# Kernel optimization log

Hardware: AMD Instinct MI355X
Metric: run time of the kernel (lower is better)

## Reference

```python
import jax, jax.numpy as jnp
import numpy as np
import math
from jax import lax

NUM_POS = 128        # random_choice in pos_neg_sampling
NUM_TOT = 256        # pos + (128 + negative_padding) always totals 256
POS_W = 10.0         # positive_weight in compute_loss


def _conv(x, w, b, pad):
    y = lax.conv_general_dilated(x, w, (1, 1), pad,
                                 dimension_numbers=('NCHW', 'OIHW', 'NCHW'))
    return y + b[None, :, None, None]


def make_anchor_box(img_h, img_w, gh, gw):
    # torch.range(0, W, W/(gw-1)) == inclusive linspace with gw points
    xs = jnp.linspace(0.0, float(img_w), gw)
    ys = jnp.linspace(0.0, float(img_h), gh)
    gx, gy = jnp.meshgrid(xs, ys, indexing='ij')          # (gw, gh) like torch.meshgrid
    xy = jnp.stack([gx.reshape(-1), gy.reshape(-1)], -1).reshape(gh, gw, 2)
    whs = []
    for area in (128 * 128, 256 * 256, 512 * 512):
        for wr, hr in ((1, 1), (2, 1), (1, 2)):
            u = math.sqrt(area / (wr * hr))
            whs.append((wr * u, hr * u))
    wh = jnp.asarray(whs, jnp.float32)                    # (9, 2)
    xy9 = jnp.broadcast_to(xy[:, :, None, :], (gh, gw, 9, 2))
    wh9 = jnp.broadcast_to(wh[None, None], (gh, gw, 9, 2))
    boxes = jnp.concatenate([xy9, xy9 + wh9], -1)         # x1,y1,x2,y2
    return boxes.reshape(-1, 4)


def pairwise_iou(t, a):
    # t: [T,4], a: [A,4], xyxy -> [T,A]
    lt = jnp.maximum(t[:, None, :2], a[None, :, :2])
    rb = jnp.minimum(t[:, None, 2:], a[None, :, 2:])
    wh = jnp.clip(rb - lt, 0.0)
    inter = wh[..., 0] * wh[..., 1]
    at = (t[:, 2] - t[:, 0]) * (t[:, 3] - t[:, 1])
    aa = (a[:, 2] - a[:, 0]) * (a[:, 3] - a[:, 1])
    return inter / (at[:, None] + aa[None, :] - inter)


def box_encode(anchor, bbox):
    awh = anchor[:, 2:] - anchor[:, :2]
    bwh = bbox[:, 2:] - bbox[:, :2]
    ac = anchor[:, :2] + awh / 2
    bc = bbox[:, :2] + bwh / 2
    dxy = (bc - ac) / awh
    dwh = jnp.log(bwh / awh)
    return jnp.concatenate([dxy, dwh], 1)


def rpn_forward(x, target, conv_w, conv_b, bbox_w, bbox_b, score_w, score_b,
                img_h, img_w):
    gh, gw = x.shape[-2], x.shape[-1]
    h = jax.nn.relu(_conv(x[None], conv_w, conv_b, 'SAME'))
    bbox = jax.nn.relu(_conv(h, bbox_w, bbox_b, 'VALID')).reshape(-1, 4)   # [A,4]
    score = jax.nn.relu(_conv(h, score_w, score_b, 'VALID')).reshape(-1, 2)  # [A,2]
    anchors = make_anchor_box(img_h, img_w, gh, gw)                        # [A,4]

    iou = pairwise_iou(target, anchors)                                    # [T,A]
    max_iou = iou.max(0)
    tgt_idx = jnp.argmax(iou, 0)

    # deterministic replacement for np.random.choice sampling (fixed shapes)
    pos_score = jnp.where(max_iou > 0.7, max_iou, -1.0)
    pos_vals, pos_idx = lax.top_k(pos_score, NUM_POS)
    pos_valid = pos_vals > 0.0
    n_pos = jnp.sum(pos_valid.astype(jnp.int32))

    neg_score = jnp.where(max_iou < 0.3, 1.0 - max_iou, -1.0)
    neg_vals, neg_idx = lax.top_k(neg_score, NUM_TOT)
    neg_valid = (neg_vals > 0.0) & (jnp.arange(NUM_TOT) < (NUM_TOT - n_pos))

    bbox_pred = bbox[pos_idx]                                              # [128,4]
    scores_sel = score[jnp.concatenate([pos_idx, neg_idx])]                # [384,2]
    valid = jnp.concatenate([pos_valid, neg_valid]).astype(jnp.float32)

    tgt_scores = jnp.concatenate([
        jnp.tile(jnp.asarray([[1.0, 0.0]], jnp.float32), (NUM_POS, 1)),
        jnp.tile(jnp.asarray([[0.0, 1.0]], jnp.float32), (NUM_TOT, 1))], 0)

    matched = target[tgt_idx[pos_idx]]
    treg = box_encode(anchors[pos_idx], matched)

    ce = -jnp.sum(tgt_scores * jax.nn.log_softmax(scores_sel, -1), -1)
    score_loss = jnp.sum(ce * valid) / jnp.maximum(jnp.sum(valid), 1.0)

    d = bbox_pred - treg
    sl1 = jnp.where(jnp.abs(d) < 1.0, 0.5 * d * d, jnp.abs(d) - 0.5)
    pm = pos_valid.astype(jnp.float32)[:, None]
    reg_loss = jnp.sum(sl1 * pm) / jnp.maximum(jnp.sum(pm) * 4.0, 1.0)

    return score_loss + POS_W * reg_loss


def setup_inputs():
    key = jax.random.key(0)
    ks = jax.random.split(key, 8)
    cin, gh, gw, nt = 512, 128, 128, 64
    x = jax.random.normal(ks[0], (cin, gh, gw), jnp.float32)
    cxy = jax.random.uniform(ks[1], (nt, 2), minval=300.0, maxval=1748.0)
    wh = jax.random.uniform(ks[2], (nt, 2), minval=64.0, maxval=512.0)
    target = jnp.concatenate([cxy - wh / 2, cxy + wh / 2], -1)
    conv_w = jax.random.normal(ks[3], (cin, cin, 3, 3), jnp.float32) * 0.02
    conv_b = jnp.zeros((cin,), jnp.float32)
    bbox_w = jax.random.normal(ks[4], (36, cin, 1, 1), jnp.float32) * 0.02
    bbox_b = jnp.zeros((36,), jnp.float32)
    score_w = jax.random.normal(ks[5], (18, cin, 1, 1), jnp.float32) * 0.02
    score_b = jnp.zeros((18,), jnp.float32)
    return {'x': x, 'target': target, 'conv_w': conv_w, 'conv_b': conv_b,
            'bbox_w': bbox_w, 'bbox_b': bbox_b, 'score_w': score_w,
            'score_b': score_b, 'img_h': 2048, 'img_w': 2048}


def reference(x, target, conv_w, conv_b, bbox_w, bbox_b, score_w, score_b,
              img_h, img_w):
    return rpn_forward(x, target, conv_w, conv_b, bbox_w, bbox_b,
                       score_w, score_b, img_h, img_w)
```

## Files before the change

kernel.cpp:

```cpp
#include <hip/hip_runtime.h>
#include <cstdint>
#include <cstddef>

typedef unsigned long long ull;
typedef __bf16 bf16x8 __attribute__((ext_vector_type(8)));
typedef float f32x4 __attribute__((ext_vector_type(4)));

#define NA     147456
#define NT     64
#define KDIM   4608
#define NTASK  1280
#define CAND_CAP 4096
#define KSPLIT 8
#define NSTEP  18
#define NIOUB  576
#define NTRB   2048
#define NPREP2 512
#define NZERO  197

#define OFF_WB2   0
#define OFF_XT    4718592
#define OFF_ZERO  22024192
#define OFF_H4    22302720
#define OFF_MIOU  43274240
#define OFF_CAND  43864064
#define OFF_CPB   45043712
#define OFF_CBZ   45046016
#define OFF_NPOS  45048320
#define OFF_TREG  45048336
#define OFF_TASKS 45050384

#define UANC 90.509667991878f
__device__ __constant__ float WKa[9] = {128.0f, 2.0f*UANC, UANC, 256.0f, 4.0f*UANC, 2.0f*UANC, 512.0f, 8.0f*UANC, 4.0f*UANC};
__device__ __constant__ float HKa[9] = {128.0f, UANC, 2.0f*UANC, 256.0f, 2.0f*UANC, 4.0f*UANC, 512.0f, 4.0f*UANC, 8.0f*UANC};

__device__ __forceinline__ float iou_one(float x1, float y1, float x2, float y2, float4 t) {
#pragma clang fp contract(off)
  float ltx = fmaxf(t.x, x1), lty = fmaxf(t.y, y1);
  float rbx = fminf(t.z, x2), rby = fminf(t.w, y2);
  float wx = fmaxf(rbx - ltx, 0.0f);
  float wy = fmaxf(rby - lty, 0.0f);
  float inter = wx * wy;
  float at = (t.z - t.x) * (t.w - t.y);
  float aa = (x2 - x1) * (y2 - y1);
  return inter / ((at + aa) - inter);
}

__device__ __forceinline__ unsigned short f2bf(float f) {
  unsigned int u = __float_as_uint(f);
  unsigned int r = (u + 0x7fffu + ((u >> 16) & 1u)) >> 16;
  return (unsigned short)r;
}

__device__ __forceinline__ int boff(int kcb) {
  int rk = kcb >> 6;
  int dy = (rk * 11) >> 5;
  int dxo = rk - dy * 3;
  return (dy * 130 + dxo) * 512 + (kcb & 63) * 8;
}

__global__ __launch_bounds__(256) void k_pi(const float* __restrict__ cw,
    unsigned short* __restrict__ Wb2, const float* __restrict__ x,
    unsigned short* __restrict__ xtb, unsigned short* __restrict__ zrg,
    const float* __restrict__ tgt, const int* __restrict__ imw,
    const int* __restrict__ imh, float* __restrict__ miou,
    ull* __restrict__ cand, int* __restrict__ cpb, int* __restrict__ cbz,
    float* __restrict__ out0) {
  __shared__ __align__(16) char smem[20480];
  int blk = blockIdx.x;
  int tid = threadIdx.x;
  if (blk >= NIOUB + NTRB + NPREP2) {
    int g = (blk - (NIOUB + NTRB + NPREP2)) * 256 + tid;
    uint4 z = {0u, 0u, 0u, 0u};
    if (g == 0) *out0 = 0.0f;
    if (g < 17408) {
      *(uint4*)(zrg + g * 8) = z;
    } else {
      int h = g - 17408;
      int pixi = h >> 6, j = h & 63;
      int yy, xx;
      if (pixi < 260) { yy = (pixi < 130) ? 0 : 129; xx = (pixi < 130) ? pixi : pixi - 130; }
      else { int p2 = pixi - 260; if (p2 < 128) { yy = 1 + p2; xx = 0; } else { yy = p2 - 127; xx = 129; } }
      *(uint4*)(xtb + (size_t)(yy * 130 + xx) * 512 + j * 8) = z;
    }
    return;
  }
  if (blk >= NIOUB + NTRB) {
    float* row = (float*)smem;
    int m = blk - (NIOUB + NTRB);
    const float* src = cw + (size_t)m * KDIM;
    for (int f = tid; f < KDIM; f += 256) {
      int cin = f / 9;
      row[cin * 10 + (f - cin * 9)] = src[f];
    }
    __syncthreads();
    for (int kc = tid; kc < 576; kc += 256) {
      int r = kc >> 6, c8 = kc & 63;
      int base = c8 * 80 + r;
      unsigned short o[8];
      #pragma unroll
      for (int j = 0; j < 8; ++j) o[j] = f2bf(row[base + j * 10]);
      *(uint4*)(Wb2 + ((size_t)kc * 512 + m) * 8) = *(const uint4*)o;
    }
    return;
  }
  if (blk >= NIOUB) {
    float* tile = (float*)smem;
    int tb = blk - NIOUB;
    int pix0 = (tb & 255) * 64;
    int cin0 = (tb >> 8) * 64;
    int pr = tid & 15, cr = tid >> 4;
    #pragma unroll
    for (int i = 0; i < 4; ++i) {
      int cin = cr + i * 16;
      float4 v = *(const float4*)(x + (size_t)(cin0 + cin) * 16384 + pix0 + pr * 4);
      tile[cin * 65 + pr * 4 + 0] = v.x;
      tile[cin * 65 + pr * 4 + 1] = v.y;
      tile[cin * 65 + pr * 4 + 2] = v.z;
      tile[cin * 65 + pr * 4 + 3] = v.w;
    }
    __syncthreads();
    #pragma unroll
    for (int i = 0; i < 4; ++i) {
      int pix = cr + i * 16;
      int plin = pix0 + pix;
      int py = plin >> 7, px = plin & 127;
      unsigned short o[4] = {f2bf(tile[(pr * 4 + 0) * 65 + pix]),
                             f2bf(tile[(pr * 4 + 1) * 65 + pix]),
                             f2bf(tile[(pr * 4 + 2) * 65 + pix]),
                             f2bf(tile[(pr * 4 + 3) * 65 + pix])};
      *(uint2*)(xtb + (size_t)((py + 1) * 130 + (px + 1)) * 512 + cin0 + pr * 4) = *(const uint2*)o;
    }
    return;
  }
  float4* ts = (float4*)smem;
  int* wz = (int*)(smem + 1024);
  int* wc = wz + 4;
  if (tid < NT) ts[tid] = ((const float4*)tgt)[tid];
  __syncthreads();
  int a = blk * 256 + tid;
  int k = a % 9;
  int pq = a / 9;
  int p = pq >> 7, q = pq & 127;
  float dx = (float)(*imw) / 127.0f;
  float dyl = (float)(*imh) / 127.0f;
  float x1 = (float)p * dx, y1 = (float)q * dyl;
  float x2 = x1 + WKa[k], y2 = y1 + HKa[k];
  float best = -1.0f;
  #pragma unroll 8
  for (int t = 0; t < NT; ++t) best = fmaxf(best, iou_one(x1, y1, x2, y2, ts[t]));
  miou[a] = best;
  int lane = tid & 63, w = tid >> 6;
  ull bz = __ballot(best == 0.0f);
  bool isc = best > 0.7f;
  ull bc = __ballot(isc);
  if (lane == 0) { wz[w] = (int)__popcll(bz); wc[w] = (int)__popcll(bc); }
  __syncthreads();
  if (tid == 0) {
    cbz[blk] = wz[0] + wz[1] + wz[2] + wz[3];
    cpb[blk] = wc[0] + wc[1] + wc[2] + wc[3];
  }
  if (isc) {
    int woff = 0;
    for (int i = 0; i < w; ++i) woff += wc[i];
    int rank = woff + (int)__popcll(bc & ((1ull << lane) - 1ull));
    cand[blk * 256 + rank] = ((ull)__float_as_uint(best) << 32) | (ull)(0xFFFFFFFFu - (unsigned)a);
  }
}

__global__ __launch_bounds__(256) void k_sel(const ull* __restrict__ cand,
    const int* __restrict__ cpb, const float* __restrict__ miou,
    const int* __restrict__ cbz, const float* __restrict__ tgt,
    const int* __restrict__ imw, const int* __restrict__ imh,
    int* __restrict__ nposp, float* __restrict__ treg, int* __restrict__ tasks) {
  __shared__ ull keys[CAND_CAP];
  __shared__ ull bnd[1024];
  __shared__ int hist[1024];
  __shared__ int cpbL[576];
  __shared__ int base576[577];
  __shared__ int wtot[4];
  __shared__ int selCnt, bndCnt, Tbin, mAbove;
  __shared__ int posi[128];
  __shared__ int npS;
  __shared__ int nzbase[145];
  __shared__ float4 ts[NT];
  __shared__ int negA[256];
  __shared__ int wsum[4];
  int tid = threadIdx.x;
  int lane = tid & 63;
  if (tid < NT) ts[tid] = ((const float4*)tgt)[tid];
  for (int i = tid; i < 576; i += 256) cpbL[i] = cpb[i];
  for (int i = tid; i < 1024; i += 256) hist[i] = 0;
  __syncthreads();
  int e0 = 0, e1 = 0, sA = 0, scanA = 0;
  if (tid < 192) {
    e0 = cpbL[3 * tid]; e1 = cpbL[3 * tid + 1]; int e2 = cpbL[3 * tid + 2];
    sA = e0 + e1 + e2;
    scanA = sA;
    for (int off = 1; off < 64; off <<= 1) {
      int v = __shfl_up(scanA, off);
      if (lane >= off) scanA += v;
    }
    if (lane == 63) wtot[tid >> 6] = scanA;
  }
  __syncthreads();
  if (tid < 192) {
    int w = tid >> 6;
    int woff = 0;
    for (int i = 0; i < w; ++i) woff += wtot[i];
    int excl = woff + scanA - sA;
    base576[3 * tid]     = excl;
    base576[3 * tid + 1] = excl + e0;
    base576[3 * tid + 2] = excl + e0 + e1;
    if (tid == 191) base576[576] = excl + sA;
  }
  __syncthreads();
  int cnt = base576[576]; if (cnt > CAND_CAP) cnt = CAND_CAP;
  for (int i = tid; i < CAND_CAP; i += 256) if (i >= cnt) keys[i] = 0ull;
  for (int rk = tid; rk < cnt; rk += 256) {
    int lo = 0, hi = 576;
    while (hi - lo > 1) { int mid = (lo + hi) >> 1; if (base576[mid] <= rk) lo = mid; else hi = mid; }
    keys[rk] = cand[lo * 256 + (rk - base576[lo])];
  }
  __syncthreads();
  if (cnt <= 128) {
    if (tid < cnt) posi[tid] = (int)(0xFFFFFFFFu - (unsigned)(keys[tid] & 0xFFFFFFFFull));
    if (tid == 0) { npS = cnt; *nposp = cnt; }
  } else {
    for (int i = tid; i < cnt; i += 256) {
      unsigned ib = (unsigned)(keys[i] >> 32);
      atomicAdd(&hist[(ib - 0x3F333334u) >> 13], 1);
    }
    __syncthreads();
    if (tid < 64) {
      int s = 0;
      #pragma unroll
      for (int t = 0; t < 16; ++t) s += hist[tid * 16 + t];
      int S = s;
      #pragma unroll
      for (int off = 1; off < 64; off <<= 1) {
        int u = __shfl_down(S, off);
        if (tid + off < 64) S += u;
      }
      ull mask = __ballot(S >= 128);
      int g = 63 - __clzll(mask);
      int aboveS = __shfl(S, (g + 1 < 64) ? g + 1 : 63);
      if (g == 63) aboveS = 0;
      if (tid == 0) {
        int run = aboveS, T = g * 16 + 15;
        for (int b = g * 16 + 15; b >= g * 16; --b) {
          int h = hist[b];
          if (run + h >= 128) { T = b; break; }
          run += h;
        }
        Tbin = T; mAbove = run; selCnt = 0; bndCnt = 0;
      }
    }
    __syncthreads();
    int T = Tbin, m = mAbove;
    for (int i = tid; i < cnt; i += 256) {
      ull kk = keys[i];
      unsigned ib = (unsigned)(kk >> 32);
      int b = (int)((ib - 0x3F333334u) >> 13);
      if (b > T) {
        int r = atomicAdd(&selCnt, 1);
        posi[r] = (int)(0xFFFFFFFFu - (unsigned)(kk & 0xFFFFFFFFull));
      } else if (b == T) {
        int r = atomicAdd(&bndCnt, 1);
        if (r < 1024) bnd[r] = kk;
      }
    }
    __syncthreads();
    int B = bndCnt;
    int need = 128 - m;
    if (B <= 1024) {
      int n2 = 2; while (n2 < B) n2 <<= 1;
      for (int i = tid; i < n2; i += 256) if (i >= B) bnd[i] = 0ull;
      for (int size = 2; size <= n2; size <<= 1)
        for (int stride = size >> 1; stride > 0; stride >>= 1) {
          __syncthreads();
          for (int t = tid; t < n2 / 2; t += 256) {
            int i = 2 * t - (t & (stride - 1));
            int j = i + stride;
            ull a = bnd[i], b2 = bnd[j];
            bool desc = ((i & size) == 0);
            if (desc ? (a < b2) : (a > b2)) { bnd[i] = b2; bnd[j] = a; }
          }
        }
      __syncthreads();
      if (tid < need) posi[m + tid] = (int)(0xFFFFFFFFu - (unsigned)(bnd[tid] & 0xFFFFFFFFull));
    } else {
      for (int size = 2; size <= CAND_CAP; size <<= 1)
        for (int stride = size >> 1; stride > 0; stride >>= 1) {
          __syncthreads();
          for (int t = tid; t < CAND_CAP / 2; t += 256) {
            int i = 2 * t - (t & (stride - 1));
            int j = i + stride;
            ull a = keys[i], b2 = keys[j];
            bool desc = ((i & size) == 0);
            if (desc ? (a < b2) : (a > b2)) { keys[i] = b2; keys[j] = a; }
          }
        }
      __syncthreads();
      if (tid < 128) posi[tid] = (int)(0xFFFFFFFFu - (unsigned)(keys[tid] & 0xFFFFFFFFull));
    }
    if (tid == 0) { npS = 128; *nposp = 128; }
  }
  __syncthreads();
  int np = npS;
  int sB = 0, scanB = 0;
  if (tid < 144) {
    int4 cz4 = *(const int4*)(cbz + 4 * tid);
    sB = cz4.x + cz4.y + cz4.z + cz4.w;
    scanB = sB;
    for (int off = 1; off < 64; off <<= 1) {
      int v = __shfl_up(scanB, off);
      if (lane >= off) scanB += v;
    }
    bool last = (tid < 128) ? (lane == 63) : (tid == 143);
    if (last) wsum[tid >> 6] = scanB;
  }
  __syncthreads();
  if (tid < 144) {
    int w = tid >> 6;
    int woff = 0;
    for (int i = 0; i < w; ++i) woff += wsum[i];
    nzbase[tid] = woff + scanB - sB;
    if (tid == 143) nzbase[144] = woff + scanB;
  }
  __syncthreads();
  int w = tid >> 6;
  for (int j = 0; j < 144; ++j) {
    if (nzbase[j] >= 256) break;
    int a0 = j * 1024 + tid * 4;
    float4 m4 = *(const float4*)(miou + a0);
    int f0 = (m4.x == 0.0f), f1 = (m4.y == 0.0f), f2 = (m4.z == 0.0f), f3 = (m4.w == 0.0f);
    int tsum = f0 + f1 + f2 + f3;
    int scan = tsum;
    for (int off = 1; off < 64; off <<= 1) {
      int v = __shfl_up(scan, off);
      if (lane >= off) scan += v;
    }
    if (lane == 63) wsum[w] = scan;
    __syncthreads();
    int woff = nzbase[j];
    for (int i = 0; i < w; ++i) woff += wsum[i];
    int r = woff + scan - tsum;
    if (f0) { if (r < 256) negA[r] = a0;     r++; }
    if (f1) { if (r < 256) negA[r] = a0 + 1; r++; }
    if (f2) { if (r < 256) negA[r] = a0 + 2; r++; }
    if (f3) { if (r < 256) negA[r] = a0 + 3;      }
    __syncthreads();
  }
  __syncthreads();
  if (tid < np) {
    int a = posi[tid];
    int k = a % 9; int pq = a / 9; int p = pq >> 7, q = pq & 127;
    float dx = (float)(*imw) / 127.0f, dyl = (float)(*imh) / 127.0f;
    float x1 = (float)p * dx, y1 = (float)q * dyl;
    float x2 = x1 + WKa[k], y2 = y1 + HKa[k];
    float best = -1.0f; int bt = 0;
    for (int t = 0; t < NT; ++t) {
      float v = iou_one(x1, y1, x2, y2, ts[t]);
      if (v > best) { best = v; bt = t; }
    }
    float4 m = ts[bt];
    float aw = x2 - x1, ah = y2 - y1;
    float acx = x1 + aw * 0.5f, acy = y1 + ah * 0.5f;
    float bwd = m.z - m.x, bhd = m.w - m.y;
    float bcx = m.x + bwd * 0.5f, bcy = m.y + bhd * 0.5f;
    treg[tid * 4 + 0] = (bcx - acx) / aw;
    treg[tid * 4 + 1] = (bcy - acy) / ah;
    treg[tid * 4 + 2] = logf(bwd / aw);
    treg[tid * 4 + 3] = logf(bhd / ah);
  }
  for (int t = tid; t < NTASK; t += 256) {
    int rec = 0;
    if (t < 768) {
      int s = t / 6, jj = t - s * 6;
      if (s < np) {
        int a = posi[s];
        int f, wr, xx;
        if (jj < 4) { f = 4 * a; wr = f >> 14; xx = (f & 127) + jj; }
        else        { f = 2 * a; wr = 36 + (f >> 14); xx = (f & 127) + (jj - 4); }
        int yy = (f >> 7) & 127;
        rec = (int)(0x80000000u | ((unsigned)wr << 16) | ((unsigned)yy << 8) | (unsigned)xx);
      }
    } else {
      int s = (t - 768) >> 1, jj = (t - 768) & 1;
      if (s < 256 - np) {
        int a = negA[s];
        int f = 2 * a; int wr = 36 + (f >> 14); int yy = (f >> 7) & 127; int xx = (f & 127) + jj;
        rec = (int)(0x80000000u | ((unsigned)wr << 16) | ((unsigned)yy << 8) | (unsigned)xx);
      }
    }
    tasks[t] = rec;
  }
}

__global__ __launch_bounds__(64) void k_mfma(const unsigned short* __restrict__ Wb2,
    const unsigned short* __restrict__ xtb, const unsigned short* __restrict__ zrg,
    const int* __restrict__ tasks, const int* __restrict__ nposp,
    float* __restrict__ H4) {
  int npos = *nposp;
  int tt0 = blockIdx.x * 64;
  int posend = 6 * npos, negend = 768 + 2 * (256 - npos);
  if (!((tt0 < posend) || ((tt0 + 64 > 768) && (tt0 < negend)))) return;
  int m_base = blockIdx.y * 64;
  int ks = blockIdx.z;
  int lane = threadIdx.x;
  int quad = lane >> 4, r = lane & 15;
  int kc0 = ks * 72 + quad;
  const bf16x8* Ab = (const bf16x8*)Wb2 + ((size_t)kc0 * 512 + m_base + r);

  const unsigned short* Bp[4];
  #pragma unroll
  for (int ni = 0; ni < 4; ++ni) {
    int rec = tasks[tt0 + ni * 16 + r];
    int pix = (rec < 0) ? (((rec >> 8) & 127) * 130 + (rec & 127)) : 0;
    const unsigned short* base = (rec < 0) ? xtb : zrg;
    Bp[ni] = base + (size_t)pix * 512 + quad * 8;
  }
  int kcb = ks * 72;

  f32x4 acc[4][4];
  #pragma unroll
  for (int i = 0; i < 4; ++i)
    #pragma unroll
    for (int j = 0; j < 4; ++j) acc[i][j] = (f32x4){0.f, 0.f, 0.f, 0.f};

  bf16x8 a[4], b[4];
  #pragma unroll
  for (int mi = 0; mi < 4; ++mi) a[mi] = Ab[mi * 16];
  int ob0 = boff(kcb);
  #pragma unroll
  for (int ni = 0; ni < 4; ++ni) b[ni] = *(const bf16x8*)(Bp[ni] + ob0);

  for (int s = 0; s < NSTEP; ++s) {
    bf16x8 an[4], bn[4];
    if (s < NSTEP - 1) {
      const bf16x8* An = Ab + (size_t)(s + 1) * 4 * 512;
      int ob = boff(kcb + 4 * (s + 1));
      #pragma unroll
      for (int mi = 0; mi < 4; ++mi) an[mi] = An[mi * 16];
      #pragma unroll
      for (int ni = 0; ni < 4; ++ni) bn[ni] = *(const bf16x8*)(Bp[ni] + ob);
    }
    #pragma unroll
    for (int mi = 0; mi < 4; ++mi)
      #pragma unroll
      for (int ni = 0; ni < 4; ++ni)
        acc[mi][ni] = __builtin_amdgcn_mfma_f32_16x16x32_bf16(a[mi], b[ni], acc[mi][ni], 0, 0, 0);
    if (s < NSTEP - 1) {
      #pragma unroll
      for (int mi = 0; mi < 4; ++mi) a[mi] = an[mi];
      #pragma unroll
      for (int ni = 0; ni < 4; ++ni) b[ni] = bn[ni];
    }
  }
  size_t hb = (size_t)ks * NTASK;
  #pragma unroll
  for (int mi = 0; mi < 4; ++mi) {
    int c = m_base + mi * 16 + quad * 4;
    #pragma unroll
    for (int ni = 0; ni < 4; ++ni) {
      int t = tt0 + ni * 16 + r;
      *(f32x4*)(H4 + (hb + t) * 512 + c) = acc[mi][ni];
    }
  }
}

__global__ __launch_bounds__(256) void k_out(const float* __restrict__ H4,
    const int* __restrict__ tasks,
    const float* __restrict__ cb, const float* __restrict__ bw,
    const float* __restrict__ bb, const float* __restrict__ sw,
    const float* __restrict__ sb, const float* __restrict__ treg,
    const int* __restrict__ nposp, float* __restrict__ out) {
  __shared__ float sOut[4];
  __shared__ float sContrib[4];
  int wave = threadIdx.x >> 6, lane = threadIdx.x & 63;
  int t = blockIdx.x * 4 + wave;
  int rec = tasks[t];
  float outval = 0.0f;
  if (rec < 0) {
    int wr = (rec >> 16) & 63;
    const float* wrow = (wr < 36) ? (bw + wr * 512) : (sw + (wr - 36) * 512);
    float s = 0.0f;
    #pragma unroll
    for (int it = 0; it < 8; ++it) {
      int c = it * 64 + lane;
      size_t o = (size_t)t * 512 + c;
      float hv = cb[c];
      #pragma unroll
      for (int kslice = 0; kslice < KSPLIT; ++kslice)
        hv += H4[o + (size_t)kslice * 1280 * 512];
      s = fmaf(fmaxf(hv, 0.0f), wrow[c], s);
    }
    #pragma unroll
    for (int off = 32; off > 0; off >>= 1) s += __shfl_down(s, off);
    if (lane == 0) {
      float b = (wr < 36) ? bb[wr] : sb[wr - 36];
      outval = fmaxf(s + b, 0.0f);
    }
  }
  if (lane == 0) sOut[wave] = outval;
  __syncthreads();
  if (lane == 0) {
    float contrib = 0.0f;
    if (rec < 0) {
      if (t < 768) {
        int s6 = t / 6, j = t - s6 * 6;
        if (j < 4) {
          int np = *nposp;
          float d = outval - treg[s6 * 4 + j];
          float ad = fabsf(d);
          float sl1 = (ad < 1.0f) ? 0.5f * d * d : ad - 0.5f;
          contrib = 10.0f * sl1 / fmaxf(4.0f * (float)np, 1.0f);
        } else if (j == 4) {
          float s0 = outval, s1 = sOut[wave + 1];
          float mm = fmaxf(s0, s1);
          float lse = mm + logf(expf(s0 - mm) + expf(s1 - mm));
          contrib = (lse - s0) * (1.0f / 256.0f);
        }
      } else if (((t - 768) & 1) == 0) {
        float s0 = outval, s1 = sOut[wave + 1];
        float mm = fmaxf(s0, s1);
        float lse = mm + logf(expf(s0 - mm) + expf(s1 - mm));
        contrib = (lse - s1) * (1.0f / 256.0f);
      }
    }
    sContrib[wave] = contrib;
  }
  __syncthreads();
  if (threadIdx.x == 0) {
    float c = sContrib[0] + sContrib[1] + sContrib[2] + sContrib[3];
    if (c != 0.0f) atomicAdd(out, c);
  }
}

extern "C" void kernel_launch(void* const* d_in, const int* in_sizes, int n_in,
                              void* d_out, int out_size, void* d_ws, size_t ws_size,
                              hipStream_t stream) {
  const float* x   = (const float*)d_in[0];
  const float* tgt = (const float*)d_in[1];
  const float* cw  = (const float*)d_in[2];
  const float* cb  = (const float*)d_in[3];
  const float* bw  = (const float*)d_in[4];
  const float* bb  = (const float*)d_in[5];
  const float* sw  = (const float*)d_in[6];
  const float* sb  = (const float*)d_in[7];
  const int* imh   = (const int*)d_in[8];
  const int* imw   = (const int*)d_in[9];

  char* ws = (char*)d_ws;
  unsigned short* Wb2 = (unsigned short*)(ws + OFF_WB2);
  unsigned short* xtb = (unsigned short*)(ws + OFF_XT);
  unsigned short* zrg = (unsigned short*)(ws + OFF_ZERO);
  float* H4    = (float*)(ws + OFF_H4);
  float* miou  = (float*)(ws + OFF_MIOU);
  ull*   cand  = (ull*)(ws + OFF_CAND);
  int*   cpb   = (int*)(ws + OFF_CPB);
  int*   cbz   = (int*)(ws + OFF_CBZ);
  int*   nposp = (int*)(ws + OFF_NPOS);
  float* treg  = (float*)(ws + OFF_TREG);
  int*   tasks = (int*)(ws + OFF_TASKS);
  float* out   = (float*)d_out;

  k_pi   <<<dim3(NIOUB + NTRB + NPREP2 + NZERO), dim3(256), 0, stream>>>(cw, Wb2, x, xtb, zrg, tgt, imw, imh, miou, cand, cpb, cbz, out);
  k_sel  <<<dim3(1),              dim3(256), 0, stream>>>(cand, cpb, miou, cbz, tgt, imw, imh, nposp, treg, tasks);
  k_mfma <<<dim3(20, 8, KSPLIT),  dim3(64),  0, stream>>>(Wb2, xtb, zrg, tasks, nposp, H4);
  k_out  <<<dim3(320),            dim3(256), 0, stream>>>(H4, tasks, cb, bw, bb, sw, sb, treg, nposp, out);
}
```

Before: 149.8 us.

## Fuse selection kernel into prep kernel via block-0 spin-wait on IoU counter

Removes the single-block k_sel launch and runs its selection logic in block 0 of k_pi. That block spin-waits on a global counter that the IoU blocks increment after a threadfence. Selection can then overlap with the transpose and weight-prep blocks of the same kernel, and one launch gap disappears. In exchange it adds a memset, reads candidate keys from global memory through a binary search on each use instead of caching them in shared memory, and relies on block 0 being co-resident with the IoU blocks to avoid deadlock.

```diff
diff --git a/kernel.cpp b/kernel.cpp
--- a/kernel.cpp
+++ b/kernel.cpp
@@ -29,6 +29,7 @@
 #define OFF_NPOS  45048320
 #define OFF_TREG  45048336
 #define OFF_TASKS 45050384
+#define OFF_CTR   45055504
 
 #define UANC 90.509667991878f
 __device__ __constant__ float WKa[9] = {128.0f, 2.0f*UANC, UANC, 256.0f, 4.0f*UANC, 2.0f*UANC, 512.0f, 8.0f*UANC, 4.0f*UANC};
@@ -59,16 +60,253 @@
   return (dy * 130 + dxo) * 512 + (kcb & 63) * 8;
 }
 
+__device__ __forceinline__ ull fetch_key(const ull* __restrict__ cand,
+                                         const int* base576, int rk) {
+  int lo = 0, hi = 576;
+  while (hi - lo > 1) { int mid = (lo + hi) >> 1; if (base576[mid] <= rk) lo = mid; else hi = mid; }
+  return cand[lo * 256 + (rk - base576[lo])];
+}
+
 __global__ __launch_bounds__(256) void k_pi(const float* __restrict__ cw,
     unsigned short* __restrict__ Wb2, const float* __restrict__ x,
     unsigned short* __restrict__ xtb, unsigned short* __restrict__ zrg,
     const float* __restrict__ tgt, const int* __restrict__ imw,
     const int* __restrict__ imh, float* __restrict__ miou,
     ull* __restrict__ cand, int* __restrict__ cpb, int* __restrict__ cbz,
-    float* __restrict__ out0) {
+    float* __restrict__ out0, int* __restrict__ nposp, float* __restrict__ treg,
+    int* __restrict__ tasks, int* __restrict__ ctr, ull* __restrict__ gscr) {
   __shared__ __align__(16) char smem[20480];
-  int blk = blockIdx.x;
+  int blk0 = blockIdx.x;
   int tid = threadIdx.x;
+
+  if (blk0 == 0) {
+    ull* bnd      = (ull*)smem;
+    int* hist     = (int*)(smem + 8192);
+    int* cpbL     = (int*)(smem + 12288);
+    int* base576  = (int*)(smem + 14592);
+    int* wtot     = (int*)(smem + 16900);
+    int* posi     = (int*)(smem + 16916);
+    int* nzbase   = (int*)(smem + 17428);
+    float4* ts    = (float4*)(smem + 18016);
+    int* negA     = (int*)(smem + 19040);
+    int* wsum     = (int*)(smem + 20064);
+    int* scal     = (int*)(smem + 20080);
+    int &selCnt = scal[0], &bndCnt = scal[1], &Tbin = scal[2], &mAbove = scal[3], &npS = scal[4];
+
+    if (tid == 0) {
+      while (atomicCAS(ctr, NIOUB, NIOUB) != NIOUB) __builtin_amdgcn_s_sleep(32);
+    }
+    __syncthreads();
+    __threadfence();
+
+    int lane = tid & 63;
+    if (tid < NT) ts[tid] = ((const float4*)tgt)[tid];
+    for (int i = tid; i < 576; i += 256) cpbL[i] = cpb[i];
+    for (int i = tid; i < 1024; i += 256) hist[i] = 0;
+    __syncthreads();
+    int e0 = 0, e1 = 0, sA = 0, scanA = 0;
+    if (tid < 192) {
+      e0 = cpbL[3 * tid]; e1 = cpbL[3 * tid + 1]; int e2 = cpbL[3 * tid + 2];
+      sA = e0 + e1 + e2;
+      scanA = sA;
+      for (int off = 1; off < 64; off <<= 1) {
+        int v = __shfl_up(scanA, off);
+        if (lane >= off) scanA += v;
+      }
+      if (lane == 63) wtot[tid >> 6] = scanA;
+    }
+    __syncthreads();
+    if (tid < 192) {
+      int w = tid >> 6;
+      int woff = 0;
+      for (int i = 0; i < w; ++i) woff += wtot[i];
+      int excl = woff + scanA - sA;
+      base576[3 * tid]     = excl;
+      base576[3 * tid + 1] = excl + e0;
+      base576[3 * tid + 2] = excl + e0 + e1;
+      if (tid == 191) base576[576] = excl + sA;
+    }
+    __syncthreads();
+    int cnt = base576[576]; if (cnt > CAND_CAP) cnt = CAND_CAP;
+    if (cnt <= 128) {
+      if (tid < cnt) posi[tid] = (int)(0xFFFFFFFFu - (unsigned)(fetch_key(cand, base576, tid) & 0xFFFFFFFFull));
+      if (tid == 0) { npS = cnt; *nposp = cnt; }
+    } else {
+      for (int i = tid; i < cnt; i += 256) {
+        unsigned ib = (unsigned)(fetch_key(cand, base576, i) >> 32);
+        atomicAdd(&hist[(ib - 0x3F333334u) >> 13], 1);
+      }
+      __syncthreads();
+      if (tid < 64) {
+        int s = 0;
+        #pragma unroll
+        for (int t = 0; t < 16; ++t) s += hist[tid * 16 + t];
+        int S = s;
+        #pragma unroll
+        for (int off = 1; off < 64; off <<= 1) {
+          int u = __shfl_down(S, off);
+          if (tid + off < 64) S += u;
+        }
+        ull mask = __ballot(S >= 128);
+        int g = 63 - __clzll(mask);
+        int aboveS = __shfl(S, (g + 1 < 64) ? g + 1 : 63);
+        if (g == 63) aboveS = 0;
+        if (tid == 0) {
+          int run = aboveS, T = g * 16 + 15;
+          for (int b = g * 16 + 15; b >= g * 16; --b) {
+            int h = hist[b];
+            if (run + h >= 128) { T = b; break; }
+            run += h;
+          }
+          Tbin = T; mAbove = run; selCnt = 0; bndCnt = 0;
+        }
+      }
+      __syncthreads();
+      int T = Tbin, m = mAbove;
+      for (int i = tid; i < cnt; i += 256) {
+        ull kk = fetch_key(cand, base576, i);
+        unsigned ib = (unsigned)(kk >> 32);
+        int b = (int)((ib - 0x3F333334u) >> 13);
+        if (b > T) {
+          int r = atomicAdd(&selCnt, 1);
+          posi[r] = (int)(0xFFFFFFFFu - (unsigned)(kk & 0xFFFFFFFFull));
+        } else if (b == T) {
+          int r = atomicAdd(&bndCnt, 1);
+          if (r < 1024) bnd[r] = kk;
+        }
+      }
+      __syncthreads();
+      int B = bndCnt;
+      int need = 128 - m;
+      if (B <= 1024) {
+        int n2 = 2; while (n2 < B) n2 <<= 1;
+        for (int i = tid; i < n2; i += 256) if (i >= B) bnd[i] = 0ull;
+        for (int size = 2; size <= n2; size <<= 1)
+          for (int stride = size >> 1; stride > 0; stride >>= 1) {
+            __syncthreads();
+            for (int t = tid; t < n2 / 2; t += 256) {
+              int i = 2 * t - (t & (stride - 1));
+              int j = i + stride;
+              ull a = bnd[i], b2 = bnd[j];
+              bool desc = ((i & size) == 0);
+              if (desc ? (a < b2) : (a > b2)) { bnd[i] = b2; bnd[j] = a; }
+            }
+          }
+        __syncthreads();
+        if (tid < need) posi[m + tid] = (int)(0xFFFFFFFFu - (unsigned)(bnd[tid] & 0xFFFFFFFFull));
+      } else {
+        for (int i = tid; i < CAND_CAP; i += 256)
+          gscr[i] = (i < cnt) ? fetch_key(cand, base576, i) : 0ull;
+        __syncthreads();
+        for (int size = 2; size <= CAND_CAP; size <<= 1)
+          for (int stride = size >> 1; stride > 0; stride >>= 1) {
+            for (int t = tid; t < CAND_CAP / 2; t += 256) {
+              int i = 2 * t - (t & (stride - 1));
+              int j = i + stride;
+              ull a = gscr[i], b2 = gscr[j];
+              bool desc = ((i & size) == 0);
+              if (desc ? (a < b2) : (a > b2)) { gscr[i] = b2; gscr[j] = a; }
+            }
+            __syncthreads();
+          }
+        if (tid < 128) posi[tid] = (int)(0xFFFFFFFFu - (unsigned)(gscr[tid] & 0xFFFFFFFFull));
+      }
+      if (tid == 0) { npS = 128; *nposp = 128; }
+    }
+    __syncthreads();
+    int np = npS;
+    int sB = 0, scanB = 0;
+    if (tid < 144) {
+      int4 cz4 = *(const int4*)(cbz + 4 * tid);
+      sB = cz4.x + cz4.y + cz4.z + cz4.w;
+      scanB = sB;
+      for (int off = 1; off < 64; off <<= 1) {
+        int v = __shfl_up(scanB, off);
+        if (lane >= off) scanB += v;
+      }
+      bool last = (tid < 128) ? (lane == 63) : (tid == 143);
+      if (last) wsum[tid >> 6] = scanB;
+    }
+    __syncthreads();
+    if (tid < 144) {
+      int w = tid >> 6;
+      int woff = 0;
+      for (int i = 0; i < w; ++i) woff += wsum[i];
+      nzbase[tid] = woff + scanB - sB;
+      if (tid == 143) nzbase[144] = woff + scanB;
+    }
+    __syncthreads();
+    int w = tid >> 6;
+    for (int j = 0; j < 144; ++j) {
+      if (nzbase[j] >= 256) break;
+      int a0 = j * 1024 + tid * 4;
+      float4 m4 = *(const float4*)(miou + a0);
+      int f0 = (m4.x == 0.0f), f1 = (m4.y == 0.0f), f2 = (m4.z == 0.0f), f3 = (m4.w == 0.0f);
+      int tsum = f0 + f1 + f2 + f3;
+      int scan = tsum;
+      for (int off = 1; off < 64; off <<= 1) {
+        int v = __shfl_up(scan, off);
+        if (lane >= off) scan += v;
+      }
+      if (lane == 63) wsum[w] = scan;
+      __syncthreads();
+      int woff = nzbase[j];
+      for (int i = 0; i < w; ++i) woff += wsum[i];
+      int r = woff + scan - tsum;
+      if (f0) { if (r < 256) negA[r] = a0;     r++; }
+      if (f1) { if (r < 256) negA[r] = a0 + 1; r++; }
+      if (f2) { if (r < 256) negA[r] = a0 + 2; r++; }
+      if (f3) { if (r < 256) negA[r] = a0 + 3;      }
+      __syncthreads();
+    }
+    __syncthreads();
+    if (tid < np) {
+      int a = posi[tid];
+      int k = a % 9; int pq = a / 9; int p = pq >> 7, q = pq & 127;
+      float dx = (float)(*imw) / 127.0f, dyl = (float)(*imh) / 127.0f;
+      float x1 = (float)p * dx, y1 = (float)q * dyl;
+      float x2 = x1 + WKa[k], y2 = y1 + HKa[k];
+      float best = -1.0f; int bt = 0;
+      for (int t = 0; t < NT; ++t) {
+        float v = iou_one(x1, y1, x2, y2, ts[t]);
+        if (v > best) { best = v; bt = t; }
+      }
+      float4 m = ts[bt];
+      float aw = x2 - x1, ah = y2 - y1;
+      float acx = x1 + aw * 0.5f, acy = y1 + ah * 0.5f;
+      float bwd = m.z - m.x, bhd = m.w - m.y;
+      float bcx = m.x + bwd * 0.5f, bcy = m.y + bhd * 0.5f;
+      treg[tid * 4 + 0] = (bcx - acx) / aw;
+      treg[tid * 4 + 1] = (bcy - acy) / ah;
+      treg[tid * 4 + 2] = logf(bwd / aw);
+      treg[tid * 4 + 3] = logf(bhd / ah);
+    }
+    for (int t = tid; t < NTASK; t += 256) {
+      int rec = 0;
+      if (t < 768) {
+        int s = t / 6, jj = t - s * 6;
+        if (s < np) {
+          int a = posi[s];
+          int f, wr, xx;
+          if (jj < 4) { f = 4 * a; wr = f >> 14; xx = (f & 127) + jj; }
+          else        { f = 2 * a; wr = 36 + (f >> 14); xx = (f & 127) + (jj - 4); }
+          int yy = (f >> 7) & 127;
+          rec = (int)(0x80000000u | ((unsigned)wr << 16) | ((unsigned)yy << 8) | (unsigned)xx);
+        }
+      } else {
+        int s = (t - 768) >> 1, jj = (t - 768) & 1;
+        if (s < 256 - np) {
+          int a = negA[s];
+          int f = 2 * a; int wr = 36 + (f >> 14); int yy = (f >> 7) & 127; int xx = (f & 127) + jj;
+          rec = (int)(0x80000000u | ((unsigned)wr << 16) | ((unsigned)yy << 8) | (unsigned)xx);
+        }
+      }
+      tasks[t] = rec;
+    }
+    return;
+  }
+
+  int blk = blk0 - 1;
   if (blk >= NIOUB + NTRB + NPREP2) {
     int g = (blk - (NIOUB + NTRB + NPREP2)) * 256 + tid;
     uint4 z = {0u, 0u, 0u, 0u};
@@ -166,236 +404,9 @@
     int rank = woff + (int)__popcll(bc & ((1ull << lane) - 1ull));
     cand[blk * 256 + rank] = ((ull)__float_as_uint(best) << 32) | (ull)(0xFFFFFFFFu - (unsigned)a);
   }
-}
-
-__global__ __launch_bounds__(256) void k_sel(const ull* __restrict__ cand,
-    const int* __restrict__ cpb, const float* __restrict__ miou,
-    const int* __restrict__ cbz, const float* __restrict__ tgt,
-    const int* __restrict__ imw, const int* __restrict__ imh,
-    int* __restrict__ nposp, float* __restrict__ treg, int* __restrict__ tasks) {
-  __shared__ ull keys[CAND_CAP];
-  __shared__ ull bnd[1024];
-  __shared__ int hist[1024];
-  __shared__ int cpbL[576];
-  __shared__ int base576[577];
-  __shared__ int wtot[4];
-  __shared__ int selCnt, bndCnt, Tbin, mAbove;
-  __shared__ int posi[128];
-  __shared__ int npS;
-  __shared__ int nzbase[145];
-  __shared__ float4 ts[NT];
-  __shared__ int negA[256];
-  __shared__ int wsum[4];
-  int tid = threadIdx.x;
-  int lane = tid & 63;
-  if (tid < NT) ts[tid] = ((const float4*)tgt)[tid];
-  for (int i = tid; i < 576; i += 256) cpbL[i] = cpb[i];
-  for (int i = tid; i < 1024; i += 256) hist[i] = 0;
+  __threadfence();
   __syncthreads();
-  int e0 = 0, e1 = 0, sA = 0, scanA = 0;
-  if (tid < 192) {
-    e0 = cpbL[3 * tid]; e1 = cpbL[3 * tid + 1]; int e2 = cpbL[3 * tid + 2];
-    sA = e0 + e1 + e2;
-    scanA = sA;
-    for (int off = 1; off < 64; off <<= 1) {
-      int v = __shfl_up(scanA, off);
-      if (lane >= off) scanA += v;
-    }
-    if (lane == 63) wtot[tid >> 6] = scanA;
-  }
-  __syncthreads();
-  if (tid < 192) {
-    int w = tid >> 6;
-    int woff = 0;
-    for (int i = 0; i < w; ++i) woff += wtot[i];
-    int excl = woff + scanA - sA;
-    base576[3 * tid]     = excl;
-    base576[3 * tid + 1] = excl + e0;
-    base576[3 * tid + 2] = excl + e0 + e1;
-    if (tid == 191) base576[576] = excl + sA;
-  }
-  __syncthreads();
-  int cnt = base576[576]; if (cnt > CAND_CAP) cnt = CAND_CAP;
-  for (int i = tid; i < CAND_CAP; i += 256) if (i >= cnt) keys[i] = 0ull;
-  for (int rk = tid; rk < cnt; rk += 256) {
-    int lo = 0, hi = 576;
-    while (hi - lo > 1) { int mid = (lo + hi) >> 1; if (base576[mid] <= rk) lo = mid; else hi = mid; }
-    keys[rk] = cand[lo * 256 + (rk - base576[lo])];
-  }
-  __syncthreads();
-  if (cnt <= 128) {
-    if (tid < cnt) posi[tid] = (int)(0xFFFFFFFFu - (unsigned)(keys[tid] & 0xFFFFFFFFull));
-    if (tid == 0) { npS = cnt; *nposp = cnt; }
-  } else {
-    for (int i = tid; i < cnt; i += 256) {
-      unsigned ib = (unsigned)(keys[i] >> 32);
-      atomicAdd(&hist[(ib - 0x3F333334u) >> 13], 1);
-    }
-    __syncthreads();
-    if (tid < 64) {
-      int s = 0;
-      #pragma unroll
-      for (int t = 0; t < 16; ++t) s += hist[tid * 16 + t];
-      int S = s;
-      #pragma unroll
-      for (int off = 1; off < 64; off <<= 1) {
-        int u = __shfl_down(S, off);
-        if (tid + off < 64) S += u;
-      }
-      ull mask = __ballot(S >= 128);
-      int g = 63 - __clzll(mask);
-      int aboveS = __shfl(S, (g + 1 < 64) ? g + 1 : 63);
-      if (g == 63) aboveS = 0;
-      if (tid == 0) {
-        int run = aboveS, T = g * 16 + 15;
-        for (int b = g * 16 + 15; b >= g * 16; --b) {
-          int h = hist[b];
-          if (run + h >= 128) { T = b; break; }
-          run += h;
-        }
-        Tbin = T; mAbove = run; selCnt = 0; bndCnt = 0;
-      }
-    }
-    __syncthreads();
-    int T = Tbin, m = mAbove;
-    for (int i = tid; i < cnt; i += 256) {
-      ull kk = keys[i];
-      unsigned ib = (unsigned)(kk >> 32);
-      int b = (int)((ib - 0x3F333334u) >> 13);
-      if (b > T) {
-        int r = atomicAdd(&selCnt, 1);
-        posi[r] = (int)(0xFFFFFFFFu - (unsigned)(kk & 0xFFFFFFFFull));
-      } else if (b == T) {
-        int r = atomicAdd(&bndCnt, 1);
-        if (r < 1024) bnd[r] = kk;
-      }
-    }
-    __syncthreads();
-    int B = bndCnt;
-    int need = 128 - m;
-    if (B <= 1024) {
-      int n2 = 2; while (n2 < B) n2 <<= 1;
-      for (int i = tid; i < n2; i += 256) if (i >= B) bnd[i] = 0ull;
-      for (int size = 2; size <= n2; size <<= 1)
-        for (int stride = size >> 1; stride > 0; stride >>= 1) {
-          __syncthreads();
-          for (int t = tid; t < n2 / 2; t += 256) {
-            int i = 2 * t - (t & (stride - 1));
-            int j = i + stride;
-            ull a = bnd[i], b2 = bnd[j];
-            bool desc = ((i & size) == 0);
-            if (desc ? (a < b2) : (a > b2)) { bnd[i] = b2; bnd[j] = a; }
-          }
-        }
-      __syncthreads();
-      if (tid < need) posi[m + tid] = (int)(0xFFFFFFFFu - (unsigned)(bnd[tid] & 0xFFFFFFFFull));
-    } else {
-      for (int size = 2; size <= CAND_CAP; size <<= 1)
-        for (int stride = size >> 1; stride > 0; stride >>= 1) {
-          __syncthreads();
-          for (int t = tid; t < CAND_CAP / 2; t += 256) {
-            int i = 2 * t - (t & (stride - 1));
-            int j = i + stride;
-            ull a = keys[i], b2 = keys[j];
-            bool desc = ((i & size) == 0);
-            if (desc ? (a < b2) : (a > b2)) { keys[i] = b2; keys[j] = a; }
-          }
-        }
-      __syncthreads();
-      if (tid < 128) posi[tid] = (int)(0xFFFFFFFFu - (unsigned)(keys[tid] & 0xFFFFFFFFull));
-    }
-    if (tid == 0) { npS = 128; *nposp = 128; }
-  }
-  __syncthreads();
-  int np = npS;
-  int sB = 0, scanB = 0;
-  if (tid < 144) {
-    int4 cz4 = *(const int4*)(cbz + 4 * tid);
-    sB = cz4.x + cz4.y + cz4.z + cz4.w;
-    scanB = sB;
-    for (int off = 1; off < 64; off <<= 1) {
-      int v = __shfl_up(scanB, off);
-      if (lane >= off) scanB += v;
-    }
-    bool last = (tid < 128) ? (lane == 63) : (tid == 143);
-    if (last) wsum[tid >> 6] = scanB;
-  }
-  __syncthreads();
-  if (tid < 144) {
-    int w = tid >> 6;
-    int woff = 0;
-    for (int i = 0; i < w; ++i) woff += wsum[i];
-    nzbase[tid] = woff + scanB - sB;
-    if (tid == 143) nzbase[144] = woff + scanB;
-  }
-  __syncthreads();
-  int w = tid >> 6;
-  for (int j = 0; j < 144; ++j) {
-    if (nzbase[j] >= 256) break;
-    int a0 = j * 1024 + tid * 4;
-    float4 m4 = *(const float4*)(miou + a0);
-    int f0 = (m4.x == 0.0f), f1 = (m4.y == 0.0f), f2 = (m4.z == 0.0f), f3 = (m4.w == 0.0f);
-    int tsum = f0 + f1 + f2 + f3;
-    int scan = tsum;
-    for (int off = 1; off < 64; off <<= 1) {
-      int v = __shfl_up(scan, off);
-      if (lane >= off) scan += v;
-    }
-    if (lane == 63) wsum[w] = scan;
-    __syncthreads();
-    int woff = nzbase[j];
-    for (int i = 0; i < w; ++i) woff += wsum[i];
-    int r = woff + scan - tsum;
-    if (f0) { if (r < 256) negA[r] = a0;     r++; }
-    if (f1) { if (r < 256) negA[r] = a0 + 1; r++; }
-    if (f2) { if (r < 256) negA[r] = a0 + 2; r++; }
-    if (f3) { if (r < 256) negA[r] = a0 + 3;      }
-    __syncthreads();
-  }
-  __syncthreads();
-  if (tid < np) {
-    int a = posi[tid];
-    int k = a % 9; int pq = a / 9; int p = pq >> 7, q = pq & 127;
-    float dx = (float)(*imw) / 127.0f, dyl = (float)(*imh) / 127.0f;
-    float x1 = (float)p * dx, y1 = (float)q * dyl;
-    float x2 = x1 + WKa[k], y2 = y1 + HKa[k];
-    float best = -1.0f; int bt = 0;
-    for (int t = 0; t < NT; ++t) {
-      float v = iou_one(x1, y1, x2, y2, ts[t]);
-      if (v > best) { best = v; bt = t; }
-    }
-    float4 m = ts[bt];
-    float aw = x2 - x1, ah = y2 - y1;
-    float acx = x1 + aw * 0.5f, acy = y1 + ah * 0.5f;
-    float bwd = m.z - m.x, bhd = m.w - m.y;
-    float bcx = m.x + bwd * 0.5f, bcy = m.y + bhd * 0.5f;
-    treg[tid * 4 + 0] = (bcx - acx) / aw;
-    treg[tid * 4 + 1] = (bcy - acy) / ah;
-    treg[tid * 4 + 2] = logf(bwd / aw);
-    treg[tid * 4 + 3] = logf(bhd / ah);
-  }
-  for (int t = tid; t < NTASK; t += 256) {
-    int rec = 0;
-    if (t < 768) {
-      int s = t / 6, jj = t - s * 6;
-      if (s < np) {
-        int a = posi[s];
-        int f, wr, xx;
-        if (jj < 4) { f = 4 * a; wr = f >> 14; xx = (f & 127) + jj; }
-        else        { f = 2 * a; wr = 36 + (f >> 14); xx = (f & 127) + (jj - 4); }
-        int yy = (f >> 7) & 127;
-        rec = (int)(0x80000000u | ((unsigned)wr << 16) | ((unsigned)yy << 8) | (unsigned)xx);
-      }
-    } else {
-      int s = (t - 768) >> 1, jj = (t - 768) & 1;
-      if (s < 256 - np) {
-        int a = negA[s];
-        int f = 2 * a; int wr = 36 + (f >> 14); int yy = (f >> 7) & 127; int xx = (f & 127) + jj;
-        rec = (int)(0x80000000u | ((unsigned)wr << 16) | ((unsigned)yy << 8) | (unsigned)xx);
-      }
-    }
-    tasks[t] = rec;
-  }
+  if (tid == 0) atomicAdd(ctr, 1);
 }
 
 __global__ __launch_bounds__(64) void k_mfma(const unsigned short* __restrict__ Wb2,
@@ -564,10 +575,13 @@
   int*   nposp = (int*)(ws + OFF_NPOS);
   float* treg  = (float*)(ws + OFF_TREG);
   int*   tasks = (int*)(ws + OFF_TASKS);
+  int*   ctr   = (int*)(ws + OFF_CTR);
   float* out   = (float*)d_out;
 
-  k_pi   <<<dim3(NIOUB + NTRB + NPREP2 + NZERO), dim3(256), 0, stream>>>(cw, Wb2, x, xtb, zrg, tgt, imw, imh, miou, cand, cpb, cbz, out);
-  k_sel  <<<dim3(1),              dim3(256), 0, stream>>>(cand, cpb, miou, cbz, tgt, imw, imh, nposp, treg, tasks);
+  hipMemsetAsync(ctr, 0, 4, stream);
+  k_pi   <<<dim3(1 + NIOUB + NTRB + NPREP2 + NZERO), dim3(256), 0, stream>>>(
+            cw, Wb2, x, xtb, zrg, tgt, imw, imh, miou, cand, cpb, cbz, out,
+            nposp, treg, tasks, ctr, (ull*)H4);
   k_mfma <<<dim3(20, 8, KSPLIT),  dim3(64),  0, stream>>>(Wb2, xtb, zrg, tasks, nposp, H4);
   k_out  <<<dim3(320),            dim3(256), 0, stream>>>(H4, tasks, cb, bw, bb, sw, sb, treg, nposp, out);
 }
```

Result: slower. 216.3 us (+44.4%).
